# Kernel optimization log

Hardware: AMD Instinct MI355X
Metric: run time of the kernel (lower is better)

The kernel has to match this reference:

```python
import jax, jax.numpy as jnp
import numpy as np

N_QUBITS = 10
N_LAYERS = 4
DIM = 2 ** N_QUBITS


def _bit(v, q, n):
    return (v >> (n - 1 - q)) & 1


def _cnot_indices(control, target, n):
    idx0, idx1 = [], []
    for i in range(2 ** n):
        if _bit(i, control, n) == 1 and _bit(i, target, n) == 0:
            idx0.append(i)
            idx1.append(i | (1 << (n - 1 - target)))
    return np.asarray(idx0, np.int32), np.asarray(idx1, np.int32)


# static precomputed CNOT swap indices for pairs (q, (q+1) % n)
_CNOT = [_cnot_indices(q, (q + 1) % N_QUBITS, N_QUBITS) for q in range(N_QUBITS)]
# Z expectation masks: [n_qubits, dim] of +/-1
_ZMASK = np.array([[1.0 - 2.0 * _bit(i, q, N_QUBITS) for i in range(DIM)]
                   for q in range(N_QUBITS)], np.float32)


def _rx(t):
    c = jnp.cos(t / 2.0).astype(jnp.complex64)
    s = jnp.sin(t / 2.0).astype(jnp.complex64)
    return jnp.stack([jnp.stack([c, -1j * s], -1),
                      jnp.stack([-1j * s, c], -1)], -2)


def _ry(t):
    c = jnp.cos(t / 2.0).astype(jnp.complex64)
    s = jnp.sin(t / 2.0).astype(jnp.complex64)
    return jnp.stack([jnp.stack([c, -s], -1),
                      jnp.stack([s, c], -1)], -2)


def _rz(t):
    tc = t.astype(jnp.complex64)
    e0 = jnp.exp(-1j * tc / 2.0)
    e1 = jnp.exp(1j * tc / 2.0)
    z = jnp.zeros_like(e0)
    return jnp.stack([jnp.stack([e0, z], -1),
                      jnp.stack([z, e1], -1)], -2)


def _apply_gate(state, gate, q):
    # state: [b, DIM] complex64; gate: [2,2] or [b,2,2]
    b = state.shape[0]
    psi = state.reshape((b,) + (2,) * N_QUBITS)
    psi = jnp.moveaxis(psi, q + 1, N_QUBITS).reshape(b, DIM // 2, 2)
    if gate.ndim == 3:
        out = jnp.einsum('bmi,bij->bmj', psi, gate)
    else:
        out = jnp.einsum('bmi,ij->bmj', psi, gate)
    out = out.reshape((b,) + (2,) * N_QUBITS)
    out = jnp.moveaxis(out, N_QUBITS, q + 1)
    return out.reshape(b, DIM)


def _cnot(state, idx0, idx1):
    return state.at[:, idx0].set(state[:, idx1]).at[:, idx1].set(state[:, idx0])


def setup_inputs() -> dict:
    key = jax.random.key(0)
    k1, k2, k3, k4 = jax.random.split(key, 4)
    x = jax.random.normal(k1, (16384, 3), jnp.float32)
    enc_W = jax.random.normal(k2, (N_QUBITS, 3), jnp.float32) * 0.3
    enc_b = jax.random.normal(k3, (N_QUBITS,), jnp.float32) * 0.1
    theta = jax.random.normal(k4, (N_LAYERS, N_QUBITS, 3), jnp.float32) * 0.04
    return {"x": x, "enc_W": enc_W, "enc_b": enc_b, "theta": theta}


def reference(x, enc_W, enc_b, theta):
    b = x.shape[0]
    enc = jnp.pi * jnp.tanh(x @ enc_W.T + enc_b)  # [b, n_qubits]
    state = jnp.zeros((b, DIM), jnp.complex64).at[:, 0].set(1.0 + 0j)
    # batched encoding RY rotations
    for q in range(N_QUBITS):
        state = _apply_gate(state, _ry(enc[:, q]), q)
    # variational layers (shared gate across batch)
    for layer in range(N_LAYERS):
        for q in range(N_QUBITS):
            state = _apply_gate(state, _rx(theta[layer, q, 0]), q)
            state = _apply_gate(state, _ry(theta[layer, q, 1]), q)
            state = _apply_gate(state, _rz(theta[layer, q, 2]), q)
        for idx0, idx1 in _CNOT:
            state = _cnot(state, idx0, idx1)
    probs = jnp.square(state.real) + jnp.square(state.imag)  # [b, DIM]
    return probs @ jnp.asarray(_ZMASK).T  # [b, n_qubits]
```

## Files before the change

kernel.cpp:

```cpp
#include <hip/hip_runtime.h>
#include <stdint.h>

#define NQ 10
#define NL 4

typedef unsigned int u32;
typedef _Float16 f16x8 __attribute__((ext_vector_type(8)));
typedef float f32x16 __attribute__((ext_vector_type(16)));
typedef u32 u32x4 __attribute__((ext_vector_type(4)));

constexpr u32 FRc(u32 r) {
    u32 r0 = r & 1, r1 = (r >> 1) & 1, r2 = (r >> 2) & 1, r3 = (r >> 3) & 1, r4 = (r >> 4) & 1;
    return (r4 << 9) | ((r3 ^ r4) << 8) | ((r2 ^ r3) << 7) | ((r1 ^ r2) << 6) |
           ((r0 ^ r1) << 5) | (r0 << 4);
}
constexpr u32 FCc(u32 c) {
    u32 c0 = c & 1, c1 = (c >> 1) & 1, c2 = (c >> 2) & 1, c3 = (c >> 3) & 1, c4 = (c >> 4) & 1;
    return (c0 << 9) | (c0 << 8) | (c4 << 4) | ((c3 ^ c4) << 3) | ((c2 ^ c3) << 2) |
           ((c1 ^ c2) << 1) | (c0 ^ c1);
}

__device__ __forceinline__ f32x16 mfma16(f16x8 a, f16x8 b, f32x16 c) {
    return __builtin_amdgcn_mfma_f32_32x32x16_f16(a, b, c, 0, 0, 0);
}
__device__ __forceinline__ f32x16 zero16() {
    f32x16 z;
#pragma unroll
    for (int i = 0; i < 16; i++) z[i] = 0.f;
    return z;
}
__device__ __forceinline__ f16x8 negf(f16x8 v) {
    u32x4 u = __builtin_bit_cast(u32x4, v);
#pragma unroll
    for (int i = 0; i < 4; i++) u[i] ^= 0x80008000u;
    return __builtin_bit_cast(f16x8, u);
}
__device__ __forceinline__ u32 pk2(float a, float b) {
    auto h = __builtin_amdgcn_cvt_pkrtz(a, b);
    return __builtin_bit_cast(u32, h);
}
__device__ __forceinline__ u32 permlo(u32 a, u32 b) { return __builtin_amdgcn_perm(b, a, 0x05040100u); }
__device__ __forceinline__ u32 permhi(u32 a, u32 b) { return __builtin_amdgcn_perm(b, a, 0x07060302u); }
__device__ __forceinline__ f16x8 mk8(u32 a, u32 b, u32 c, u32 d) {
    u32x4 v; v[0] = a; v[1] = b; v[2] = c; v[3] = d;
    return __builtin_bit_cast(f16x8, v);
}
template <int MASK>
__device__ __forceinline__ float swz(float v) {
    return __int_as_float(__builtin_amdgcn_ds_swizzle(__float_as_int(v), (MASK << 10) | 0x1F));
}
__device__ __forceinline__ u32 bpermu(int addr, u32 v) {
    return (u32)__builtin_amdgcn_ds_bpermute(addr, (int)v);
}
__device__ __forceinline__ void cmulh(float ar, float ai, float br, float bi, float& cr, float& ci) {
    cr = ar * br - ai * bi;
    ci = ar * bi + ai * br;
}

__device__ __forceinline__ void c2a(const f32x16& V, bool hb, int addr32, u32 (&o)[8]) {
    u32 pw[8];
#pragma unroll
    for (int p = 0; p < 8; p++) pw[p] = pk2(V[2 * p], V[2 * p + 1]);
    u32 s0 = hb ? pw[0] : pw[2];
    u32 s1 = hb ? pw[1] : pw[3];
    u32 s2 = hb ? pw[4] : pw[6];
    u32 s3 = hb ? pw[5] : pw[7];
    u32 r0 = bpermu(addr32, s0), r1 = bpermu(addr32, s1);
    u32 r2 = bpermu(addr32, s2), r3 = bpermu(addr32, s3);
    o[0] = hb ? r0 : pw[0]; o[1] = hb ? r1 : pw[1];
    o[2] = hb ? pw[2] : r0; o[3] = hb ? pw[3] : r1;
    o[4] = hb ? r2 : pw[4]; o[5] = hb ? r3 : pw[5];
    o[6] = hb ? pw[6] : r2; o[7] = hb ? pw[7] : r3;
}

__global__ __launch_bounds__(256) void tq_all(
    const float* __restrict__ x, const float* __restrict__ encW,
    const float* __restrict__ encb, const float* __restrict__ theta,
    float* __restrict__ out, int batch) {
    __shared__ u32 pool[13120];
    const int tid = threadIdx.x;
    float* gp = (float*)(pool + 12800);
    float2* K4p = (float2*)(pool + 8704);

    if (tid < NL * NQ) {
        float hx = 0.5f * theta[tid * 3 + 0];
        float hy = 0.5f * theta[tid * 3 + 1];
        float hz = 0.5f * theta[tid * 3 + 2];
        float cx = cosf(hx), sx = sinf(hx);
        float cy = cosf(hy), sy = sinf(hy);
        float cz = cosf(hz), sz = sinf(hz);
        float m00r = cx * cy, m00i = -sx * sy;
        float m01r = -cx * sy, m01i = -sx * cy;
        float m10r = cx * sy, m10i = -sx * cy;
        float m11r = cx * cy, m11i = sx * sy;
        float g00r, g00i, g01r, g01i, g10r, g10i, g11r, g11i;
        cmulh(m00r, m00i, cz, -sz, g00r, g00i);
        cmulh(m10r, m10i, cz, -sz, g10r, g10i);
        cmulh(m01r, m01i, cz, sz, g01r, g01i);
        cmulh(m11r, m11i, cz, sz, g11r, g11i);
        float* o = gp + tid * 8;
        o[0] = g00r; o[1] = g00i; o[2] = g01r; o[3] = g01i;
        o[4] = g10r; o[5] = g10i; o[6] = g11r; o[7] = g11i;
    }
    if (tid < 128) {
        int lane = tid & 63, kh = tid >> 6;
        int q = lane & 31, hf = (lane >> 5) & 1;
        u32 M = (q == 0) ? 0xFu : (q == 1) ? 0x18u : (q == 2) ? 0x1Cu : (q == 3) ? 0x1Eu : 0x1Fu;
        u32 w[4];
#pragma unroll
        for (int p = 0; p < 4; p++) {
            int k0 = kh * 16 + hf * 8 + 2 * p, k1 = k0 + 1;
            float v0 = (__builtin_popcount((u32)k0 & M) & 1) ? -1.f : 1.f;
            float v1 = (__builtin_popcount((u32)k1 & M) & 1) ? -1.f : 1.f;
            w[p] = pk2(v0, v1);
        }
        u32x4 v4; v4[0] = w[0]; v4[1] = w[1]; v4[2] = w[2]; v4[3] = w[3];
        *(u32x4*)(pool + (32 + kh) * 256 + lane * 4) = v4;
    }
    __syncthreads();
#pragma unroll 1
    for (int rr = 0; rr < 8; rr++) {
        int e = rr * 256 + tid;
        int lm = e >> 8, idx = e & 255, k = idx >> 4, m = idx & 15;
        int gb = (lm >> 1) * 10 + (lm & 1) * 5;
        float pr = 1.f, pi = 0.f;
#pragma unroll
        for (int u = 0; u < 4; u++) {
            const float* gg = gp + (gb + u) * 8;
            int bi = (k >> (3 - u)) & 1, bo = (m >> (3 - u)) & 1;
            float er = gg[(bi * 2 + bo) * 2 + 0], ei = gg[(bi * 2 + bo) * 2 + 1];
            float nr, ni;
            cmulh(pr, pi, er, ei, nr, ni);
            pr = nr; pi = ni;
        }
        K4p[lm * 256 + idx] = make_float2(pr, pi);
    }
    __syncthreads();
#pragma unroll 1
    for (int rr = 0; rr < 4; rr++) {
        int t = rr * 256 + tid;
        int lane = t & 63, kh = (t >> 6) & 1, lm = t >> 7;
        int m = lane & 31, hf = (lane >> 5) & 1;
        int gb = (lm >> 1) * 10 + (lm & 1) * 5;
        const float* g4 = gp + (gb + 4) * 8;
        int mu = m & 1;
        float e0r = g4[mu * 2 + 0], e0i = g4[mu * 2 + 1];
        float e1r = g4[(2 + mu) * 2 + 0], e1i = g4[(2 + mu) * 2 + 1];
        float2 kv[4];
#pragma unroll
        for (int jj = 0; jj < 4; jj++)
            kv[jj] = K4p[lm * 256 + (kh * 8 + hf * 4 + jj) * 16 + (m >> 1)];
        float vr[8], vi[8];
#pragma unroll
        for (int j = 0; j < 8; j++) {
            float2 a = kv[j >> 1];
            float er = (j & 1) ? e1r : e0r, ei = (j & 1) ? e1i : e0i;
            cmulh(a.x, a.y, er, ei, vr[j], vi[j]);
        }
        u32x4 wre, wim;
#pragma unroll
        for (int p = 0; p < 4; p++) {
            wre[p] = pk2(vr[2 * p], vr[2 * p + 1]);
            wim[p] = pk2(vi[2 * p], vi[2 * p + 1]);
        }
        *(u32x4*)(pool + (lm * 4 + kh) * 256 + lane * 4) = wre;
        *(u32x4*)(pool + (lm * 4 + 2 + kh) * 256 + lane * 4) = wim;
    }
    __syncthreads();

    int wave = blockIdx.x * 4 + (tid >> 6);
    int lane = tid & 63;
    if (wave >= batch) return;
    u32* slab = pool + 8704 + (tid >> 6) * 1024;
    const int col = lane & 31;
    const int half_ = lane >> 5;
    const bool hb = half_ != 0;
    const int addr32 = (lane ^ 32) << 2;
    const u32 Fc5 = FCc((u32)col);

    float x0 = x[wave * 3 + 0], x1 = x[wave * 3 + 1], x2 = x[wave * 3 + 2];
    float hc = 1.f, hs = 0.f;
    if (lane < NQ) {
        float tta = 3.14159265358979323846f *
                    tanhf(x0 * encW[lane * 3 + 0] + x1 * encW[lane * 3 + 1] +
                          x2 * encW[lane * 3 + 2] + encb[lane]);
        float h = 0.5f * tta;
        hc = cosf(h);
        hs = sinf(h);
    }
    float fcv[NQ], fsv[NQ];
#pragma unroll
    for (int q = 0; q < NQ; q++) {
        fcv[q] = __shfl(hc, q, 64);
        fsv[q] = __shfl(hs, q, 64);
    }
    float colf = 1.f;
    colf *= ((col >> 4) & 1) ? -fsv[5] : fcv[5];
    colf *= ((col >> 3) & 1) ? -fsv[6] : fcv[6];
    colf *= ((col >> 2) & 1) ? -fsv[7] : fcv[7];
    colf *= ((col >> 1) & 1) ? -fsv[8] : fcv[8];
    colf *= (col & 1) ? -fsv[9] : fcv[9];
    float f1h = half_ ? -fsv[1] : fcv[1];
    float gj[8];
#pragma unroll
    for (int j = 0; j < 8; j++) {
        gj[j] = ((j & 4) ? -fsv[2] : fcv[2]) * ((j & 2) ? -fsv[3] : fcv[3]) *
                ((j & 1) ? -fsv[4] : fcv[4]);
    }
    f16x8 Sr0, Sr1, Si0, Si1;
#pragma unroll
    for (int j = 0; j < 8; j++) {
        Sr0[j] = (_Float16)(fcv[0] * f1h * gj[j] * colf);
        Sr1[j] = (_Float16)(-fsv[0] * f1h * gj[j] * colf);
        Si0[j] = (_Float16)0.f;
        Si1[j] = (_Float16)0.f;
    }

    const f16x8* FR = (const f16x8*)pool;
    f32x16 Ur, Ui;
#pragma unroll
    for (int l = 0; l < NL; l++) {
        f16x8 Wr0 = FR[(8 * l + 0) * 64 + lane], Wr1 = FR[(8 * l + 1) * 64 + lane];
        f16x8 Wi0 = FR[(8 * l + 2) * 64 + lane], Wi1 = FR[(8 * l + 3) * 64 + lane];
        f16x8 Vr0 = FR[(8 * l + 4) * 64 + lane], Vr1 = FR[(8 * l + 5) * 64 + lane];
        f16x8 Vi0 = FR[(8 * l + 6) * 64 + lane], Vi1 = FR[(8 * l + 7) * 64 + lane];

        f32x16 Tr = zero16(), Ti = zero16();
        Tr = mfma16(Sr0, Wr0, Tr);
        Tr = mfma16(Sr1, Wr1, Tr);
        Ti = mfma16(Sr0, Wi0, Ti);
        Ti = mfma16(Sr1, Wi1, Ti);
        if (l > 0) {
            f16x8 nSi0 = negf(Si0), nSi1 = negf(Si1);
            Tr = mfma16(nSi0, Wi0, Tr);
            Tr = mfma16(nSi1, Wi1, Tr);
            Ti = mfma16(Si0, Wr0, Ti);
            Ti = mfma16(Si1, Wr1, Ti);
        }

        u32 oR[8], oI[8];
        c2a(Tr, hb, addr32, oR);
        c2a(Ti, hb, addr32, oI);
        f16x8 TAr0 = mk8(oR[0], oR[1], oR[2], oR[3]);
        f16x8 TAr1 = mk8(oR[4], oR[5], oR[6], oR[7]);
        f16x8 TAi0 = mk8(oI[0], oI[1], oI[2], oI[3]);
        f16x8 TAi1 = mk8(oI[4], oI[5], oI[6], oI[7]);

        Ur = zero16();
        Ui = zero16();
        Ur = mfma16(TAr0, Vr0, Ur);
        Ur = mfma16(TAr1, Vr1, Ur);
        {
            f16x8 nTAi0 = negf(TAi0), nTAi1 = negf(TAi1);
            Ur = mfma16(nTAi0, Vi0, Ur);
            Ur = mfma16(nTAi1, Vi1, Ur);
        }
        Ui = mfma16(TAr0, Vi0, Ui);
        Ui = mfma16(TAr1, Vi1, Ui);
        Ui = mfma16(TAi0, Vr0, Ui);
        Ui = mfma16(TAi1, Vr1, Ui);

        if (l < NL - 1) {
            {
                u32* wb = slab + col + half_ * (4 * 32);
#pragma unroll
                for (int gi = 0; gi < 16; gi++) {
                    int rb = (gi & 3) + 8 * (gi >> 2);
                    wb[rb * 32] = pk2(Ur[gi], Ui[gi]);
                }
            }
            u32 sb[16];
            {
                u32 fh = Fc5 ^ (half_ ? FRc(8) : 0u);
#pragma unroll
                for (int kh = 0; kh < 2; kh++)
#pragma unroll
                    for (int j = 0; j < 8; j++)
                        sb[kh * 8 + j] = slab[FRc(kh * 16 + j) ^ fh];
            }
            Sr0 = mk8(permlo(sb[0], sb[1]), permlo(sb[2], sb[3]),
                      permlo(sb[4], sb[5]), permlo(sb[6], sb[7]));
            Sr1 = mk8(permlo(sb[8], sb[9]), permlo(sb[10], sb[11]),
                      permlo(sb[12], sb[13]), permlo(sb[14], sb[15]));
            Si0 = mk8(permhi(sb[0], sb[1]), permhi(sb[2], sb[3]),
                      permhi(sb[4], sb[5]), permhi(sb[6], sb[7]));
            Si1 = mk8(permhi(sb[8], sb[9]), permhi(sb[10], sb[11]),
                      permhi(sb[12], sb[13]), permhi(sb[14], sb[15]));
        }
    }

    f32x16 P;
#pragma unroll
    for (int gi = 0; gi < 16; gi++) P[gi] = Ur[gi] * Ur[gi] + Ui[gi] * Ui[gi];
    u32 po[8];
    c2a(P, hb, addr32, po);
    f16x8 PB0 = mk8(po[0], po[1], po[2], po[3]);
    f16x8 PB1 = mk8(po[4], po[5], po[6], po[7]);
    f16x8 Srw0 = FR[32 * 64 + lane], Srw1 = FR[33 * 64 + lane];
    f32x16 D = mfma16(Srw0, PB0, mfma16(Srw1, PB1, zero16()));

    u32 b4 = (col >> 4) & 1, b3 = (col >> 3) & 1, b2 = (col >> 2) & 1,
        b1 = (col >> 1) & 1, b0 = col & 1;
    u32 p4 = b4, p43 = p4 ^ b3, p432 = p43 ^ b2, p4321 = p432 ^ b1, pall = p4321 ^ b0;
    u32 sg[6];
    sg[0] = hb ? 0u : pall;
    sg[1] = hb ? p4 : 0u;
    sg[2] = hb ? p43 : 0u;
    sg[3] = hb ? p432 : 0u;
    sg[4] = hb ? 0u : p4321;
    sg[5] = hb ? 0u : pall;
    float red[6];
#pragma unroll
    for (int s = 0; s < 6; s++) {
        float v = __uint_as_float(__float_as_uint(D[s]) ^ (sg[s] << 31));
        v += swz<1>(v);
        v += swz<2>(v);
        v += swz<4>(v);
        v += swz<8>(v);
        v += swz<16>(v);
        red[s] = v;
    }
    int cc = col - ((col >= 4) ? 4 : 0);
    float v = red[0];
    v = (cc == 1) ? red[1] : v;
    v = (cc == 2) ? red[2] : v;
    v = (cc == 3) ? red[3] : v;
    v = (cc == 4) ? red[4] : v;
    v = (cc == 5) ? red[5] : v;
    bool st = hb ? (col >= 4 && col < 8) : (col < 4 || col == 8 || col == 9);
    if (st) out[wave * NQ + col] = v;
}

extern "C" void kernel_launch(void* const* d_in, const int* in_sizes, int n_in,
                              void* d_out, int out_size, void* d_ws, size_t ws_size,
                              hipStream_t stream) {
    const float* x = (const float*)d_in[0];
    const float* encW = (const float*)d_in[1];
    const float* encb = (const float*)d_in[2];
    const float* th = (const float*)d_in[3];
    float* out = (float*)d_out;
    int batch = in_sizes[0] / 3;
    int blocks = (batch + 3) / 4;
    tq_all<<<blocks, 256, 0, stream>>>(x, encW, encb, th, out, batch);
}
```

Baseline: 113.7 us.

## Split gate-fragment precompute into a separate prep kernel read from global memory

Before, every block recomputed the per-layer 32x32 gate matrices (as f16 MFMA fragments) in shared memory, with three barriers, ahead of its own simulation. Now a small prep kernel computes those fragments once into the workspace, and the main kernel loads them straight from global memory (likely served from cache) with a much smaller shared allocation and no prep barriers. This removes redundant per-block trig and matrix-building work and may improve occupancy, at the cost of an extra launch and global/L2 fragment loads in the inner loop.

```diff
diff --git a/kernel.cpp b/kernel.cpp
--- a/kernel.cpp
+++ b/kernel.cpp
@@ -73,19 +73,13 @@
     o[6] = hb ? pw[6] : r2; o[7] = hb ? pw[7] : r3;
 }
 
-__global__ __launch_bounds__(256) void tq_all(
-    const float* __restrict__ x, const float* __restrict__ encW,
-    const float* __restrict__ encb, const float* __restrict__ theta,
-    float* __restrict__ out, int batch) {
-    __shared__ u32 pool[13120];
-    const int tid = threadIdx.x;
-    float* gp = (float*)(pool + 12800);
-    float2* K4p = (float2*)(pool + 8704);
-
-    if (tid < NL * NQ) {
-        float hx = 0.5f * theta[tid * 3 + 0];
-        float hy = 0.5f * theta[tid * 3 + 1];
-        float hz = 0.5f * theta[tid * 3 + 2];
+__global__ void tq_prep(const float* __restrict__ theta, uint16_t* __restrict__ frag) {
+    __shared__ float g[NL * NQ][8];
+    int tt = threadIdx.x;
+    if (tt < NL * NQ) {
+        float hx = 0.5f * theta[tt * 3 + 0];
+        float hy = 0.5f * theta[tt * 3 + 1];
+        float hz = 0.5f * theta[tt * 3 + 2];
         float cx = cosf(hx), sx = sinf(hx);
         float cy = cosf(hy), sy = sinf(hy);
         float cz = cosf(hz), sz = sinf(hz);
@@ -98,80 +92,59 @@
         cmulh(m10r, m10i, cz, -sz, g10r, g10i);
         cmulh(m01r, m01i, cz, sz, g01r, g01i);
         cmulh(m11r, m11i, cz, sz, g11r, g11i);
-        float* o = gp + tid * 8;
-        o[0] = g00r; o[1] = g00i; o[2] = g01r; o[3] = g01i;
-        o[4] = g10r; o[5] = g10i; o[6] = g11r; o[7] = g11i;
-    }
-    if (tid < 128) {
-        int lane = tid & 63, kh = tid >> 6;
-        int q = lane & 31, hf = (lane >> 5) & 1;
-        u32 M = (q == 0) ? 0xFu : (q == 1) ? 0x18u : (q == 2) ? 0x1Cu : (q == 3) ? 0x1Eu : 0x1Fu;
-        u32 w[4];
-#pragma unroll
-        for (int p = 0; p < 4; p++) {
-            int k0 = kh * 16 + hf * 8 + 2 * p, k1 = k0 + 1;
-            float v0 = (__builtin_popcount((u32)k0 & M) & 1) ? -1.f : 1.f;
-            float v1 = (__builtin_popcount((u32)k1 & M) & 1) ? -1.f : 1.f;
-            w[p] = pk2(v0, v1);
-        }
-        u32x4 v4; v4[0] = w[0]; v4[1] = w[1]; v4[2] = w[2]; v4[3] = w[3];
-        *(u32x4*)(pool + (32 + kh) * 256 + lane * 4) = v4;
+        g[tt][0] = g00r; g[tt][1] = g00i; g[tt][2] = g01r; g[tt][3] = g01i;
+        g[tt][4] = g10r; g[tt][5] = g10i; g[tt][6] = g11r; g[tt][7] = g11i;
     }
     __syncthreads();
-#pragma unroll 1
-    for (int rr = 0; rr < 8; rr++) {
-        int e = rr * 256 + tid;
-        int lm = e >> 8, idx = e & 255, k = idx >> 4, m = idx & 15;
-        int gb = (lm >> 1) * 10 + (lm & 1) * 5;
+    int t = blockIdx.x * blockDim.x + tt;
+    int lane = t & 63, kh = (t >> 6) & 1, part = (t >> 7) & 1, mat = (t >> 8) & 1, l = t >> 9;
+    int mn = lane & 31, hf = (lane >> 5) & 1;
+#pragma unroll
+    for (int j = 0; j < 8; j++) {
+        int k = kh * 16 + hf * 8 + j;
         float pr = 1.f, pi = 0.f;
 #pragma unroll
-        for (int u = 0; u < 4; u++) {
-            const float* gg = gp + (gb + u) * 8;
-            int bi = (k >> (3 - u)) & 1, bo = (m >> (3 - u)) & 1;
-            float er = gg[(bi * 2 + bo) * 2 + 0], ei = gg[(bi * 2 + bo) * 2 + 1];
+        for (int u = 0; u < 5; u++) {
+            int q = mat ? (5 + u) : u;
+            int bi_ = (k >> (4 - u)) & 1;
+            int bo_ = (mn >> (4 - u)) & 1;
+            const float* gg = g[l * NQ + q];
+            float er = gg[(bi_ * 2 + bo_) * 2 + 0];
+            float ei = gg[(bi_ * 2 + bo_) * 2 + 1];
             float nr, ni;
             cmulh(pr, pi, er, ei, nr, ni);
-            pr = nr; pi = ni;
-        }
-        K4p[lm * 256 + idx] = make_float2(pr, pi);
-    }
-    __syncthreads();
-#pragma unroll 1
-    for (int rr = 0; rr < 4; rr++) {
-        int t = rr * 256 + tid;
-        int lane = t & 63, kh = (t >> 6) & 1, lm = t >> 7;
-        int m = lane & 31, hf = (lane >> 5) & 1;
-        int gb = (lm >> 1) * 10 + (lm & 1) * 5;
-        const float* g4 = gp + (gb + 4) * 8;
-        int mu = m & 1;
-        float e0r = g4[mu * 2 + 0], e0i = g4[mu * 2 + 1];
-        float e1r = g4[(2 + mu) * 2 + 0], e1i = g4[(2 + mu) * 2 + 1];
-        float2 kv[4];
-#pragma unroll
-        for (int jj = 0; jj < 4; jj++)
-            kv[jj] = K4p[lm * 256 + (kh * 8 + hf * 4 + jj) * 16 + (m >> 1)];
-        float vr[8], vi[8];
+            pr = nr;
+            pi = ni;
+        }
+        float v = part ? pi : pr;
+        _Float16 h = (_Float16)v;
+        frag[t * 8 + j] = __builtin_bit_cast(unsigned short, h);
+    }
+    if (blockIdx.x == 0 && tt < 128) {
+        int ln = tt & 63, kh2 = tt >> 6;
+        int q = ln & 31, hf2 = (ln >> 5) & 1;
+        u32 M = (q == 0) ? 0xFu : (q == 1) ? 0x18u : (q == 2) ? 0x1Cu : (q == 3) ? 0x1Eu : 0x1Fu;
+        uint16_t* o = frag + ((32 + kh2) * 64 + ln) * 8;
 #pragma unroll
         for (int j = 0; j < 8; j++) {
-            float2 a = kv[j >> 1];
-            float er = (j & 1) ? e1r : e0r, ei = (j & 1) ? e1i : e0i;
-            cmulh(a.x, a.y, er, ei, vr[j], vi[j]);
-        }
-        u32x4 wre, wim;
-#pragma unroll
-        for (int p = 0; p < 4; p++) {
-            wre[p] = pk2(vr[2 * p], vr[2 * p + 1]);
-            wim[p] = pk2(vi[2 * p], vi[2 * p + 1]);
-        }
-        *(u32x4*)(pool + (lm * 4 + kh) * 256 + lane * 4) = wre;
-        *(u32x4*)(pool + (lm * 4 + 2 + kh) * 256 + lane * 4) = wim;
-    }
-    __syncthreads();
-
-    int wave = blockIdx.x * 4 + (tid >> 6);
+            int k = kh2 * 16 + hf2 * 8 + j;
+            float v = (__builtin_popcount((u32)k & M) & 1) ? -1.f : 1.f;
+            _Float16 h = (_Float16)v;
+            o[j] = __builtin_bit_cast(unsigned short, h);
+        }
+    }
+}
+
+__global__ __launch_bounds__(256) void tq_main(
+    const float* __restrict__ x, const float* __restrict__ encW,
+    const float* __restrict__ encb, const uint16_t* __restrict__ frag,
+    float* __restrict__ out, int batch) {
+    __shared__ u32 smem[4 * 1024];
+    int tid = threadIdx.x;
+    int wave = (blockIdx.x * blockDim.x + tid) >> 6;
     int lane = tid & 63;
     if (wave >= batch) return;
-    u32* slab = pool + 8704 + (tid >> 6) * 1024;
+    u32* slab = smem + (tid >> 6) * 1024;
     const int col = lane & 31;
     const int half_ = lane >> 5;
     const bool hb = half_ != 0;
@@ -216,14 +189,16 @@
         Si1[j] = (_Float16)0.f;
     }
 
-    const f16x8* FR = (const f16x8*)pool;
+    const f16x8* fr = (const f16x8*)frag;
+#define FRAG(f) fr[((f)*64) + lane]
+
     f32x16 Ur, Ui;
 #pragma unroll
     for (int l = 0; l < NL; l++) {
-        f16x8 Wr0 = FR[(8 * l + 0) * 64 + lane], Wr1 = FR[(8 * l + 1) * 64 + lane];
-        f16x8 Wi0 = FR[(8 * l + 2) * 64 + lane], Wi1 = FR[(8 * l + 3) * 64 + lane];
-        f16x8 Vr0 = FR[(8 * l + 4) * 64 + lane], Vr1 = FR[(8 * l + 5) * 64 + lane];
-        f16x8 Vi0 = FR[(8 * l + 6) * 64 + lane], Vi1 = FR[(8 * l + 7) * 64 + lane];
+        f16x8 Wr0 = FRAG(8 * l + 0), Wr1 = FRAG(8 * l + 1);
+        f16x8 Wi0 = FRAG(8 * l + 2), Wi1 = FRAG(8 * l + 3);
+        f16x8 Vr0 = FRAG(8 * l + 4), Vr1 = FRAG(8 * l + 5);
+        f16x8 Vi0 = FRAG(8 * l + 6), Vi1 = FRAG(8 * l + 7);
 
         f32x16 Tr = zero16(), Ti = zero16();
         Tr = mfma16(Sr0, Wr0, Tr);
@@ -296,7 +271,7 @@
     c2a(P, hb, addr32, po);
     f16x8 PB0 = mk8(po[0], po[1], po[2], po[3]);
     f16x8 PB1 = mk8(po[4], po[5], po[6], po[7]);
-    f16x8 Srw0 = FR[32 * 64 + lane], Srw1 = FR[33 * 64 + lane];
+    f16x8 Srw0 = FRAG(32), Srw1 = FRAG(33);
     f32x16 D = mfma16(Srw0, PB0, mfma16(Srw1, PB1, zero16()));
 
     u32 b4 = (col >> 4) & 1, b3 = (col >> 3) & 1, b2 = (col >> 2) & 1,
@@ -339,7 +314,10 @@
     const float* encb = (const float*)d_in[2];
     const float* th = (const float*)d_in[3];
     float* out = (float*)d_out;
+    uint16_t* frag = (uint16_t*)d_ws;
     int batch = in_sizes[0] / 3;
-    int blocks = (batch + 3) / 4;
-    tq_all<<<blocks, 256, 0, stream>>>(x, encW, encb, th, out, batch);
-}
+
+    tq_prep<<<2, 1024, 0, stream>>>(th, frag);
+    int total_threads = batch * 64;
+    tq_main<<<(total_threads + 255) / 256, 256, 0, stream>>>(x, encW, encb, frag, out, batch);
+}
```

New measurement: 102.6 us. 9.8% less time.
